# Kernel optimization log

Measured on AMD Instinct MI355X. Metric: run time of the kernel, lower is better.

## Reference

```python
import jax, jax.numpy as jnp
import numpy as np

N_NODES = 50000
N_EDGES = 800000
HEADS = 4
NEG_SLOPE = 0.2  # DGL GATConv default and act1 slope


def _gat_layer(x, src, dst, W, al, ar, b, n_nodes, heads, dh):
    # x: [N, Fin] -> proj: [N, H, Dh]
    proj = (x @ W).reshape(n_nodes, heads, dh)
    el = jnp.einsum('nhd,hd->nh', proj, al)  # [N, H]
    er = jnp.einsum('nhd,hd->nh', proj, ar)  # [N, H]
    e = jax.nn.leaky_relu(el[src] + er[dst], NEG_SLOPE)  # [E, H]
    # segment softmax over incoming edges of each dst node
    m = jax.ops.segment_max(e, dst, num_segments=n_nodes)
    m = jnp.where(jnp.isfinite(m), m, jnp.zeros_like(m))
    ex = jnp.exp(e - m[dst])
    s = jax.ops.segment_sum(ex, dst, num_segments=n_nodes)
    alpha = ex / (s[dst] + 1e-9)  # [E, H]
    msg = proj[src] * alpha[:, :, None]  # [E, H, Dh]
    out = jax.ops.segment_sum(msg, dst, num_segments=n_nodes)  # [N, H, Dh]
    return out.reshape(n_nodes, heads * dh) + b


def setup_inputs() -> dict:
    key = jax.random.key(0)
    ks = jax.random.split(key, 10)
    d = {
        'init_emb': jax.random.normal(ks[0], (N_NODES, 300), jnp.float32) * 0.1,
        'W1': jax.random.normal(ks[1], (300, 400), jnp.float32) * (1.0 / np.sqrt(300)),
        'al1': jax.random.normal(ks[2], (HEADS, 100), jnp.float32) * 0.1,
        'ar1': jax.random.normal(ks[3], (HEADS, 100), jnp.float32) * 0.1,
        'b1': jnp.zeros((400,), jnp.float32),
        'W2': jax.random.normal(ks[4], (400, 512), jnp.float32) * (1.0 / np.sqrt(400)),
        'al2': jax.random.normal(ks[5], (HEADS, 128), jnp.float32) * 0.1,
        'ar2': jax.random.normal(ks[6], (HEADS, 128), jnp.float32) * 0.1,
        'b2': jnp.zeros((512,), jnp.float32),
        'src': jax.random.randint(ks[7], (N_EDGES,), 0, N_NODES, jnp.int32),
        'dst': jax.random.randint(ks[8], (N_EDGES,), 0, N_NODES, jnp.int32),
    }
    return d


def reference(init_emb, W1, al1, ar1, b1, W2, al2, ar2, b2, src, dst):
    x = _gat_layer(init_emb, src, dst, W1, al1, ar1, b1, N_NODES, HEADS, 100)  # [N, 400]
    x = jax.nn.leaky_relu(x, NEG_SLOPE)  # act1
    x = _gat_layer(x, src, dst, W2, al2, ar2, b2, N_NODES, HEADS, 128)  # [N, 512]
    return x
```

## Files before the change

### kernel.cpp

```cpp
#include <hip/hip_runtime.h>
#include <math.h>
#include <stdint.h>

#define NN 50000
#define NE 800000
#define HEADS 4
#define MPAD 50048

typedef __attribute__((ext_vector_type(8))) short bf16x8;
typedef __attribute__((ext_vector_type(4))) float f32x4;

__device__ __forceinline__ uint32_t bf16rne(float x) {
  uint32_t b = __float_as_uint(x);
  return (b + 0x7FFFu + ((b >> 16) & 1u)) >> 16;
}
__device__ __forceinline__ float bflo(uint32_t v) {
  return __uint_as_float(v << 16);
}
__device__ __forceinline__ float bfhi(uint32_t v) {
  return __uint_as_float(v & 0xFFFF0000u);
}

__global__ void hist_kernel(const int* __restrict__ dst, int* __restrict__ counts, int n) {
  int i = blockIdx.x * blockDim.x + threadIdx.x;
  if (i < n) atomicAdd(&counts[dst[i]], 1);
}

__global__ void scan_kernel(const int* __restrict__ counts, int* __restrict__ row_ptr, int n) {
  __shared__ int wsum[16];
  const int lane = threadIdx.x & 63;
  const int w = threadIdx.x >> 6;
  int carry = 0;
  for (int start = 0; start < n; start += 1024) {
    int i = start + (int)threadIdx.x;
    int v = (i < n) ? counts[i] : 0;
    int x = v;
#pragma unroll
    for (int off = 1; off < 64; off <<= 1) {
      int t = __shfl_up(x, off);
      if (lane >= off) x += t;
    }
    if (lane == 63) wsum[w] = x;
    __syncthreads();
    if (w == 0 && lane < 16) {
      int s = wsum[lane];
#pragma unroll
      for (int off = 1; off < 16; off <<= 1) {
        int t = __shfl_up(s, off);
        if (lane >= off) s += t;
      }
      wsum[lane] = s;
    }
    __syncthreads();
    int woff = (w > 0) ? wsum[w - 1] : 0;
    int incl = x + woff;
    if (i < n) row_ptr[i] = carry + incl - v;
    carry += wsum[15];
    __syncthreads();
  }
  if (threadIdx.x == 0) row_ptr[n] = carry;
}

__global__ void scatter_kernel(const int* __restrict__ dst, const int* __restrict__ src,
                               const int* __restrict__ row_ptr, int* __restrict__ cursor,
                               int* __restrict__ srcs, int n) {
  int i = blockIdx.x * blockDim.x + threadIdx.x;
  if (i < n) {
    int d = dst[i];
    int pos = atomicAdd(&cursor[d], 1);
    srcs[row_ptr[d] + pos] = src[i];
  }
}

__global__ void presplit_pairs(const float* __restrict__ X, unsigned short* __restrict__ X2,
                               int M, int K, int ksteps) {
  const int m = blockIdx.y;
  const int t = threadIdx.x;
  if (t >= ksteps * 4) return;
  const int s = t >> 2, q = t & 3;
  const int kb = s * 32 + q * 8;
  float v[8];
#pragma unroll
  for (int j = 0; j < 8; ++j) {
    int k = kb + j;
    v[j] = (m < M && k < K) ? X[(size_t)m * K + k] : 0.f;
  }
  uint32_t hi[8], lo[8];
#pragma unroll
  for (int j = 0; j < 8; ++j) {
    hi[j] = bf16rne(v[j]);
    float back = __uint_as_float(hi[j] << 16);
    lo[j] = bf16rne(v[j] - back);
  }
  uint4 hp, lp;
  hp.x = hi[0] | (hi[1] << 16);
  hp.y = hi[2] | (hi[3] << 16);
  hp.z = hi[4] | (hi[5] << 16);
  hp.w = hi[6] | (hi[7] << 16);
  lp.x = lo[0] | (lo[1] << 16);
  lp.y = lo[2] | (lo[3] << 16);
  lp.z = lo[4] | (lo[5] << 16);
  lp.w = lo[6] | (lo[7] << 16);
  char* rowp = (char*)X2 + (size_t)m * (ksteps * 128) + s * 128;
  const int x = m & 7;
  *(uint4*)(rowp + ((q ^ x) << 4)) = hp;
  *(uint4*)(rowp + (((4 | q) ^ x) << 4)) = lp;
}

__global__ void presplit_pairs_b(const float* __restrict__ W, unsigned short* __restrict__ B2,
                                 int K, int N, int ksteps) {
  const int n = blockIdx.y;
  const int t = threadIdx.x;
  if (t >= ksteps * 4) return;
  const int s = t >> 2, q = t & 3;
  const int kb = s * 32 + q * 8;
  float v[8];
#pragma unroll
  for (int j = 0; j < 8; ++j) {
    int k = kb + j;
    v[j] = (n < N && k < K) ? W[(size_t)k * N + n] : 0.f;
  }
  uint32_t hi[8], lo[8];
#pragma unroll
  for (int j = 0; j < 8; ++j) {
    hi[j] = bf16rne(v[j]);
    float back = __uint_as_float(hi[j] << 16);
    lo[j] = bf16rne(v[j] - back);
  }
  uint4 hp, lp;
  hp.x = hi[0] | (hi[1] << 16);
  hp.y = hi[2] | (hi[3] << 16);
  hp.z = hi[4] | (hi[5] << 16);
  hp.w = hi[6] | (hi[7] << 16);
  lp.x = lo[0] | (lo[1] << 16);
  lp.y = lo[2] | (lo[3] << 16);
  lp.z = lo[4] | (lo[5] << 16);
  lp.w = lo[6] | (lo[7] << 16);
  char* rowp = (char*)B2 + (size_t)n * (ksteps * 128) + s * 128;
  const int x = n & 7;
  *(uint4*)(rowp + ((q ^ x) << 4)) = hp;
  *(uint4*)(rowp + (((4 | q) ^ x) << 4)) = lp;
}

__global__ __launch_bounds__(256, 2) void gemm_pairs(
    const unsigned short* __restrict__ A2, const unsigned short* __restrict__ B2,
    unsigned short* __restrict__ Ch, int M, int ksteps, int NstR, int RSc,
    int DHR, int DHP, int magic) {
  __shared__ unsigned short As[8192];
  __shared__ unsigned short Bs[8192];
  const int tid = threadIdx.x;
  const int w = tid >> 6, lane = tid & 63;
  const int wr = w >> 1, wc = w & 1;
  const int ln = lane & 15, quad = lane >> 4;
  const int m0 = blockIdx.y * 128, n0 = blockIdx.x * 128;
  const long strideB = (long)ksteps * 128;

  f32x4 acc[4][4];
#pragma unroll
  for (int mi = 0; mi < 4; ++mi)
#pragma unroll
    for (int ni = 0; ni < 4; ++ni) acc[mi][ni] = (f32x4){0.f, 0.f, 0.f, 0.f};

  const int xa = ln & 7;
  const int gA0 = (quad ^ xa) << 4, gA1 = ((4 | quad) ^ xa) << 4;

  for (int s = 0; s < ksteps; ++s) {
    const long sb = (long)s * 128;
#pragma unroll
    for (int j = 0; j < 4; ++j) {
      const int t16 = w * 4 + j;
      const int row = t16 * 8 + (lane >> 3);
      const int gran = lane & 7;
      const char* gpA = (const char*)A2 + (size_t)(m0 + row) * strideB + sb + gran * 16;
      const char* gpB = (const char*)B2 + (size_t)(n0 + row) * strideB + sb + gran * 16;
      __builtin_amdgcn_global_load_lds(
          (const __attribute__((address_space(1))) void*)gpA,
          (__attribute__((address_space(3))) void*)((char*)As + t16 * 1024), 16, 0, 0);
      __builtin_amdgcn_global_load_lds(
          (const __attribute__((address_space(1))) void*)gpB,
          (__attribute__((address_space(3))) void*)((char*)Bs + t16 * 1024), 16, 0, 0);
    }
    __syncthreads();
    bf16x8 ah[4], alo[4], bh[4], blo[4];
#pragma unroll
    for (int mi = 0; mi < 4; ++mi) {
      const int rA = wr * 64 + mi * 16 + ln;
      ah[mi] = *(const bf16x8*)((const char*)As + rA * 128 + gA0);
      alo[mi] = *(const bf16x8*)((const char*)As + rA * 128 + gA1);
    }
#pragma unroll
    for (int ni = 0; ni < 4; ++ni) {
      const int rB = wc * 64 + ni * 16 + ln;
      bh[ni] = *(const bf16x8*)((const char*)Bs + rB * 128 + gA0);
      blo[ni] = *(const bf16x8*)((const char*)Bs + rB * 128 + gA1);
    }
#pragma unroll
    for (int mi = 0; mi < 4; ++mi)
#pragma unroll
      for (int ni = 0; ni < 4; ++ni)
        acc[mi][ni] = __builtin_amdgcn_mfma_f32_16x16x32_bf16(ah[mi], bh[ni], acc[mi][ni], 0, 0, 0);
#pragma unroll
    for (int mi = 0; mi < 4; ++mi)
#pragma unroll
      for (int ni = 0; ni < 4; ++ni)
        acc[mi][ni] = __builtin_amdgcn_mfma_f32_16x16x32_bf16(ah[mi], blo[ni], acc[mi][ni], 0, 0, 0);
#pragma unroll
    for (int mi = 0; mi < 4; ++mi)
#pragma unroll
      for (int ni = 0; ni < 4; ++ni)
        acc[mi][ni] = __builtin_amdgcn_mfma_f32_16x16x32_bf16(alo[mi], bh[ni], acc[mi][ni], 0, 0, 0);
    __syncthreads();
  }
#pragma unroll
  for (int mi = 0; mi < 4; ++mi) {
#pragma unroll
    for (int r = 0; r < 4; ++r) {
      int gm = m0 + wr * 64 + mi * 16 + quad * 4 + r;
      if (gm < M) {
        unsigned short* crow = Ch + (size_t)gm * RSc;
#pragma unroll
        for (int ni = 0; ni < 4; ++ni) {
          int gn = n0 + wc * 64 + ni * 16 + ln;
          if (gn < NstR) {
            int h = (gn * magic) >> 12;
            int col = h * DHP + (gn - h * DHR);
            crow[col] = (unsigned short)bf16rne(acc[mi][ni][r]);
          }
        }
      }
    }
  }
}

template <int DHR, int DHP>
__global__ void el_er_kernel(const unsigned short* __restrict__ projh,
                             const float* __restrict__ al, const float* __restrict__ ar,
                             float* __restrict__ el, float* __restrict__ er) {
  int t = blockIdx.x * blockDim.x + threadIdx.x;
  if (t >= NN * HEADS) return;
  int h = t & (HEADS - 1);
  int n = t >> 2;
  const unsigned short* pr = projh + (size_t)n * (HEADS * DHP) + (size_t)h * DHP;
  const float* alh = al + h * DHR;
  const float* arh = ar + h * DHR;
  float sl = 0.f, sr = 0.f;
#pragma unroll 4
  for (int d = 0; d < DHR; d += 4) {
    uint2 pv = *(const uint2*)&pr[d];
    float p0 = bflo(pv.x), p1 = bfhi(pv.x), p2 = bflo(pv.y), p3 = bfhi(pv.y);
    float4 av = *(const float4*)&alh[d];
    float4 rv = *(const float4*)&arh[d];
    sl += p0 * av.x + p1 * av.y + p2 * av.z + p3 * av.w;
    sr += p0 * rv.x + p1 * rv.y + p2 * rv.z + p3 * rv.w;
  }
  el[t] = sl;
  er[t] = sr;
}

template <int DHP, int DHR, bool ACT>
__global__ __launch_bounds__(256) void aggregate2(
    const unsigned short* __restrict__ projh, const float* __restrict__ el,
    const float* __restrict__ er, const float* __restrict__ bias,
    const int* __restrict__ row_ptr, const int* __restrict__ srcs,
    float* __restrict__ out) {
  constexpr int LPH = DHP / 8;
  constexpr int RS = HEADS * DHP * 2;
  const int node = blockIdx.x * 4 + (threadIdx.x >> 6);
  if (node >= NN) return;
  const int lane = threadIdx.x & 63;
  const int beg = row_ptr[node], end = row_ptr[node + 1];
  const int e16 = lane >> 2, hp = lane & 3;
  const float er_p = er[node * 4 + hp];
  int head;
  if constexpr (LPH == 16) head = lane >> 4;
  else head = (lane * 5) >> 6;
  const int u = lane - head * LPH;
  const int laneByte = head * (DHP * 2) + u * 16;
  const bool active = lane < 4 * LPH;
  const char* pb = (const char*)projh;

  float bv[8];
  const int d0 = u * 8;
#pragma unroll
  for (int j = 0; j < 8; ++j)
    bv[j] = (active && d0 + j < DHR) ? bias[head * DHR + d0 + j] : 0.f;

  float acc[8];
#pragma unroll
  for (int j = 0; j < 8; ++j) acc[j] = 0.f;
  float lsum = 0.f;

  int i = beg;
  int rem = end - beg;
  int sE = 0;
  float elv = 0.f;
  if (rem > 0 && e16 < rem) {
    sE = srcs[i + e16];
    elv = el[sE * 4 + hp];
  }
  while (rem > 0) {
    const int take = rem < 16 ? rem : 16;
    float ev = elv + er_p;
    ev = fmaxf(ev, 0.2f * ev);
    const float pv_ = (e16 < take) ? __expf(ev) : 0.f;
    const int off_ = sE * RS;
    const int i2 = i + take;
    const int rem2 = rem - take;
    int sEn = 0;
    float elvn = 0.f;
    if (rem2 > 0 && e16 < rem2) {
      sEn = srcs[i2 + e16];
      elvn = el[sEn * 4 + hp];
    }
    if (take == 16) {
#pragma unroll
      for (int e = 0; e < 16; ++e) {
        const int sl = e * 4 + head;
        const float pv = __shfl(pv_, sl);
        const int off = __shfl(off_, sl);
        uint4 q = *(const uint4*)(pb + (uint32_t)(off + laneByte));
        lsum += pv;
        acc[0] += pv * bflo(q.x);
        acc[1] += pv * bfhi(q.x);
        acc[2] += pv * bflo(q.y);
        acc[3] += pv * bfhi(q.y);
        acc[4] += pv * bflo(q.z);
        acc[5] += pv * bfhi(q.z);
        acc[6] += pv * bflo(q.w);
        acc[7] += pv * bfhi(q.w);
      }
    } else {
      for (int e = 0; e < take; ++e) {
        const int sl = e * 4 + head;
        const float pv = __shfl(pv_, sl);
        const int off = __shfl(off_, sl);
        uint4 q = *(const uint4*)(pb + (uint32_t)(off + laneByte));
        lsum += pv;
        acc[0] += pv * bflo(q.x);
        acc[1] += pv * bfhi(q.x);
        acc[2] += pv * bflo(q.y);
        acc[3] += pv * bfhi(q.y);
        acc[4] += pv * bflo(q.z);
        acc[5] += pv * bfhi(q.z);
        acc[6] += pv * bflo(q.w);
        acc[7] += pv * bfhi(q.w);
      }
    }
    sE = sEn;
    elv = elvn;
    i = i2;
    rem = rem2;
  }

  const float inv = 1.f / (lsum + 1e-9f);
  if (active) {
    float o[8];
#pragma unroll
    for (int j = 0; j < 8; ++j) {
      float v = acc[j] * inv + bv[j];
      if (ACT) v = (v > 0.f) ? v : 0.2f * v;
      o[j] = v;
    }
    float* orow = out + (size_t)node * (HEADS * DHR) + head * DHR + d0;
    *(float4*)orow = make_float4(o[0], o[1], o[2], o[3]);
    if (d0 + 7 < DHR) *(float4*)(orow + 4) = make_float4(o[4], o[5], o[6], o[7]);
  }
}

extern "C" void kernel_launch(void* const* d_in, const int* in_sizes, int n_in,
                              void* d_out, int out_size, void* d_ws, size_t ws_size,
                              hipStream_t stream) {
  const float* init_emb = (const float*)d_in[0];
  const float* W1 = (const float*)d_in[1];
  const float* al1 = (const float*)d_in[2];
  const float* ar1 = (const float*)d_in[3];
  const float* b1 = (const float*)d_in[4];
  const float* W2 = (const float*)d_in[5];
  const float* al2 = (const float*)d_in[6];
  const float* ar2 = (const float*)d_in[7];
  const float* b2 = (const float*)d_in[8];
  const int* src = (const int*)d_in[9];
  const int* dst = (const int*)d_in[10];
  float* out = (float*)d_out;

  char* ws = (char*)d_ws;
  size_t off = 0;
  auto alloc = [&](size_t bytes) {
    void* p = ws + off;
    off += (bytes + 255) & ~((size_t)255);
    return p;
  };
  unsigned short* projh = (unsigned short*)alloc((size_t)NN * 512 * 2);
  float* x1 = (float*)alloc((size_t)NN * 400 * 4);
  float* el = (float*)alloc((size_t)NN * HEADS * 4);
  float* er = (float*)alloc((size_t)NN * HEADS * 4);
  unsigned short* B2 = (unsigned short*)alloc((size_t)512 * 13 * 128);
  int* row_ptr = (int*)alloc((size_t)(NN + 1) * 4);
  int* counts = (int*)alloc((size_t)NN * 4);
  int* srcs = (int*)alloc((size_t)NE * 4);
  unsigned short* A2 = (unsigned short*)d_out;

  hipMemsetAsync(counts, 0, (size_t)NN * 4, stream);
  hist_kernel<<<(NE + 255) / 256, 256, 0, stream>>>(dst, counts, NE);
  scan_kernel<<<1, 1024, 0, stream>>>(counts, row_ptr, NN);
  hipMemsetAsync(counts, 0, (size_t)NN * 4, stream);
  scatter_kernel<<<(NE + 255) / 256, 256, 0, stream>>>(dst, src, row_ptr, counts, srcs, NE);

  presplit_pairs<<<dim3(1, MPAD), 64, 0, stream>>>(init_emb, A2, NN, 300, 10);
  presplit_pairs_b<<<dim3(1, 512), 64, 0, stream>>>(W1, B2, 300, 400, 10);
  gemm_pairs<<<dim3(4, MPAD / 128), 256, 0, stream>>>(A2, B2, projh, NN, 10, 400, 416, 100, 104, 41);
  el_er_kernel<100, 104><<<(NN * HEADS + 255) / 256, 256, 0, stream>>>(projh, al1, ar1, el, er);
  aggregate2<104, 100, true><<<(NN + 3) / 4, 256, 0, stream>>>(projh, el, er, b1, row_ptr, srcs, x1);

  presplit_pairs<<<dim3(1, MPAD), 64, 0, stream>>>(x1, A2, NN, 400, 13);
  presplit_pairs_b<<<dim3(1, 512), 64, 0, stream>>>(W2, B2, 400, 512, 13);
  gemm_pairs<<<dim3(4, MPAD / 128), 256, 0, stream>>>(A2, B2, projh, NN, 13, 512, 512, 128, 128, 32);
  el_er_kernel<128, 128><<<(NN * HEADS + 255) / 256, 256, 0, stream>>>(projh, al2, ar2, el, er);
  aggregate2<128, 128, false><<<(NN + 3) / 4, 256, 0, stream>>>(projh, el, er, b2, row_ptr, srcs, out);
}
```

Baseline: 797.4 us.

## Fuse layer-1 output bf16 split into aggregation and repack W2 for padded heads

```diff
diff --git a/kernel.cpp b/kernel.cpp
--- a/kernel.cpp
+++ b/kernel.cpp
@@ -73,38 +73,42 @@
 }
 
 __global__ void presplit_pairs(const float* __restrict__ X, unsigned short* __restrict__ X2,
-                               int M, int K, int ksteps) {
-  const int m = blockIdx.y;
-  const int t = threadIdx.x;
-  if (t >= ksteps * 4) return;
+                               int M, int Mpad, int K, int ksteps) {
+  const int wid = blockIdx.x * (blockDim.x >> 6) + (threadIdx.x >> 6);
+  const int nw = gridDim.x * (blockDim.x >> 6);
+  const int t = threadIdx.x & 63;
   const int s = t >> 2, q = t & 3;
+  const bool act = t < ksteps * 4;
   const int kb = s * 32 + q * 8;
-  float v[8];
-#pragma unroll
-  for (int j = 0; j < 8; ++j) {
-    int k = kb + j;
-    v[j] = (m < M && k < K) ? X[(size_t)m * K + k] : 0.f;
-  }
-  uint32_t hi[8], lo[8];
-#pragma unroll
-  for (int j = 0; j < 8; ++j) {
-    hi[j] = bf16rne(v[j]);
-    float back = __uint_as_float(hi[j] << 16);
-    lo[j] = bf16rne(v[j] - back);
-  }
-  uint4 hp, lp;
-  hp.x = hi[0] | (hi[1] << 16);
-  hp.y = hi[2] | (hi[3] << 16);
-  hp.z = hi[4] | (hi[5] << 16);
-  hp.w = hi[6] | (hi[7] << 16);
-  lp.x = lo[0] | (lo[1] << 16);
-  lp.y = lo[2] | (lo[3] << 16);
-  lp.z = lo[4] | (lo[5] << 16);
-  lp.w = lo[6] | (lo[7] << 16);
-  char* rowp = (char*)X2 + (size_t)m * (ksteps * 128) + s * 128;
-  const int x = m & 7;
-  *(uint4*)(rowp + ((q ^ x) << 4)) = hp;
-  *(uint4*)(rowp + (((4 | q) ^ x) << 4)) = lp;
+  for (int m = wid; m < Mpad; m += nw) {
+    if (!act) continue;
+    float v[8];
+#pragma unroll
+    for (int j = 0; j < 8; ++j) {
+      int k = kb + j;
+      v[j] = (m < M && k < K) ? X[(size_t)m * K + k] : 0.f;
+    }
+    uint32_t hi[8], lo[8];
+#pragma unroll
+    for (int j = 0; j < 8; ++j) {
+      hi[j] = bf16rne(v[j]);
+      float back = __uint_as_float(hi[j] << 16);
+      lo[j] = bf16rne(v[j] - back);
+    }
+    uint4 hp, lp;
+    hp.x = hi[0] | (hi[1] << 16);
+    hp.y = hi[2] | (hi[3] << 16);
+    hp.z = hi[4] | (hi[5] << 16);
+    hp.w = hi[6] | (hi[7] << 16);
+    lp.x = lo[0] | (lo[1] << 16);
+    lp.y = lo[2] | (lo[3] << 16);
+    lp.z = lo[4] | (lo[5] << 16);
+    lp.w = lo[6] | (lo[7] << 16);
+    char* rowp = (char*)X2 + (size_t)m * (ksteps * 128) + s * 128;
+    const int x = m & 7;
+    *(uint4*)(rowp + ((q ^ x) << 4)) = hp;
+    *(uint4*)(rowp + (((4 | q) ^ x) << 4)) = lp;
+  }
 }
 
 __global__ void presplit_pairs_b(const float* __restrict__ W, unsigned short* __restrict__ B2,
@@ -137,6 +141,42 @@
   lp.z = lo[4] | (lo[5] << 16);
   lp.w = lo[6] | (lo[7] << 16);
   char* rowp = (char*)B2 + (size_t)n * (ksteps * 128) + s * 128;
+  const int x = n & 7;
+  *(uint4*)(rowp + ((q ^ x) << 4)) = hp;
+  *(uint4*)(rowp + (((4 | q) ^ x) << 4)) = lp;
+}
+
+__global__ void presplit_pairs_b2(const float* __restrict__ W, unsigned short* __restrict__ B2) {
+  const int n = blockIdx.y;
+  const int t = threadIdx.x;
+  if (t >= 52) return;
+  const int s = t >> 2, q = t & 3;
+  const int kb = s * 32 + q * 8;
+  float v[8];
+#pragma unroll
+  for (int j = 0; j < 8; ++j) {
+    int kp = kb + j;
+    int h = kp / 104;
+    int d = kp - h * 104;
+    v[j] = (d < 100) ? W[(size_t)(h * 100 + d) * 512 + n] : 0.f;
+  }
+  uint32_t hi[8], lo[8];
+#pragma unroll
+  for (int j = 0; j < 8; ++j) {
+    hi[j] = bf16rne(v[j]);
+    float back = __uint_as_float(hi[j] << 16);
+    lo[j] = bf16rne(v[j] - back);
+  }
+  uint4 hp, lp;
+  hp.x = hi[0] | (hi[1] << 16);
+  hp.y = hi[2] | (hi[3] << 16);
+  hp.z = hi[4] | (hi[5] << 16);
+  hp.w = hi[6] | (hi[7] << 16);
+  lp.x = lo[0] | (lo[1] << 16);
+  lp.y = lo[2] | (lo[3] << 16);
+  lp.z = lo[4] | (lo[5] << 16);
+  lp.w = lo[6] | (lo[7] << 16);
+  char* rowp = (char*)B2 + (size_t)n * 1664 + s * 128;
   const int x = n & 7;
   *(uint4*)(rowp + ((q ^ x) << 4)) = hp;
   *(uint4*)(rowp + (((4 | q) ^ x) << 4)) = lp;
@@ -257,12 +297,12 @@
   er[t] = sr;
 }
 
-template <int DHP, int DHR, bool ACT>
+template <int DHP, int DHR, bool ACT, bool EMIT>
 __global__ __launch_bounds__(256) void aggregate2(
     const unsigned short* __restrict__ projh, const float* __restrict__ el,
     const float* __restrict__ er, const float* __restrict__ bias,
     const int* __restrict__ row_ptr, const int* __restrict__ srcs,
-    float* __restrict__ out) {
+    float* __restrict__ out, unsigned short* __restrict__ a2) {
   constexpr int LPH = DHP / 8;
   constexpr int RS = HEADS * DHP * 2;
   const int node = blockIdx.x * 4 + (threadIdx.x >> 6);
@@ -275,8 +315,8 @@
   if constexpr (LPH == 16) head = lane >> 4;
   else head = (lane * 5) >> 6;
   const int u = lane - head * LPH;
-  const int laneByte = head * (DHP * 2) + u * 16;
   const bool active = lane < 4 * LPH;
+  const int laneByte = active ? head * (DHP * 2) + u * 16 : 0;
   const char* pb = (const char*)projh;
 
   float bv[8];
@@ -359,11 +399,35 @@
     for (int j = 0; j < 8; ++j) {
       float v = acc[j] * inv + bv[j];
       if (ACT) v = (v > 0.f) ? v : 0.2f * v;
-      o[j] = v;
-    }
-    float* orow = out + (size_t)node * (HEADS * DHR) + head * DHR + d0;
-    *(float4*)orow = make_float4(o[0], o[1], o[2], o[3]);
-    if (d0 + 7 < DHR) *(float4*)(orow + 4) = make_float4(o[4], o[5], o[6], o[7]);
+      o[j] = (d0 + j < DHR) ? v : 0.f;
+    }
+    if constexpr (EMIT) {
+      uint32_t hi8[8], lo8[8];
+#pragma unroll
+      for (int j = 0; j < 8; ++j) {
+        hi8[j] = bf16rne(o[j]);
+        float back = __uint_as_float(hi8[j] << 16);
+        lo8[j] = bf16rne(o[j] - back);
+      }
+      uint4 hpx, lpx;
+      hpx.x = hi8[0] | (hi8[1] << 16);
+      hpx.y = hi8[2] | (hi8[3] << 16);
+      hpx.z = hi8[4] | (hi8[5] << 16);
+      hpx.w = hi8[6] | (hi8[7] << 16);
+      lpx.x = lo8[0] | (lo8[1] << 16);
+      lpx.y = lo8[2] | (lo8[3] << 16);
+      lpx.z = lo8[4] | (lo8[5] << 16);
+      lpx.w = lo8[6] | (lo8[7] << 16);
+      const int kp = head * DHP + u * 8;
+      const int s2 = kp >> 5, q2 = (kp >> 3) & 3, xs = node & 7;
+      char* rb = (char*)a2 + (size_t)node * 1664 + s2 * 128;
+      *(uint4*)(rb + ((q2 ^ xs) << 4)) = hpx;
+      *(uint4*)(rb + (((4 | q2) ^ xs) << 4)) = lpx;
+    } else {
+      float* orow = out + (size_t)node * (HEADS * DHR) + head * DHR + d0;
+      *(float4*)orow = make_float4(o[0], o[1], o[2], o[3]);
+      if (d0 + 7 < DHR) *(float4*)(orow + 4) = make_float4(o[4], o[5], o[6], o[7]);
+    }
   }
 }
 
@@ -391,7 +455,6 @@
     return p;
   };
   unsigned short* projh = (unsigned short*)alloc((size_t)NN * 512 * 2);
-  float* x1 = (float*)alloc((size_t)NN * 400 * 4);
   float* el = (float*)alloc((size_t)NN * HEADS * 4);
   float* er = (float*)alloc((size_t)NN * HEADS * 4);
   unsigned short* B2 = (unsigned short*)alloc((size_t)512 * 13 * 128);
@@ -406,15 +469,16 @@
   hipMemsetAsync(counts, 0, (size_t)NN * 4, stream);
   scatter_kernel<<<(NE + 255) / 256, 256, 0, stream>>>(dst, src, row_ptr, counts, srcs, NE);
 
-  presplit_pairs<<<dim3(1, MPAD), 64, 0, stream>>>(init_emb, A2, NN, 300, 10);
+  presplit_pairs<<<1024, 256, 0, stream>>>(init_emb, A2, NN, MPAD, 300, 10);
   presplit_pairs_b<<<dim3(1, 512), 64, 0, stream>>>(W1, B2, 300, 400, 10);
   gemm_pairs<<<dim3(4, MPAD / 128), 256, 0, stream>>>(A2, B2, projh, NN, 10, 400, 416, 100, 104, 41);
   el_er_kernel<100, 104><<<(NN * HEADS + 255) / 256, 256, 0, stream>>>(projh, al1, ar1, el, er);
-  aggregate2<104, 100, true><<<(NN + 3) / 4, 256, 0, stream>>>(projh, el, er, b1, row_ptr, srcs, x1);
-
-  presplit_pairs<<<dim3(1, MPAD), 64, 0, stream>>>(x1, A2, NN, 400, 13);
-  presplit_pairs_b<<<dim3(1, 512), 64, 0, stream>>>(W2, B2, 400, 512, 13);
+  aggregate2<104, 100, true, true><<<(NN + 3) / 4, 256, 0, stream>>>(projh, el, er, b1, row_ptr,
+                                                                     srcs, nullptr, A2);
+
+  presplit_pairs_b2<<<dim3(1, 512), 64, 0, stream>>>(W2, B2);
   gemm_pairs<<<dim3(4, MPAD / 128), 256, 0, stream>>>(A2, B2, projh, NN, 13, 512, 512, 128, 128, 32);
   el_er_kernel<128, 128><<<(NN * HEADS + 255) / 256, 256, 0, stream>>>(projh, al2, ar2, el, er);
-  aggregate2<128, 128, false><<<(NN + 3) / 4, 256, 0, stream>>>(projh, el, er, b2, row_ptr, srcs, out);
-}
+  aggregate2<128, 128, false, false><<<(NN + 3) / 4, 256, 0, stream>>>(projh, el, er, b2, row_ptr,
+                                                                       srcs, out, nullptr);
+}
```

New measurement: 774.4 us. -2.9%, faster.

## Fuse layer-1 aggregation with bf16 pair split and merge preprocessing kernels

Applied to the files above, without the earlier changes.

```diff
diff --git a/kernel.cpp b/kernel.cpp
--- a/kernel.cpp
+++ b/kernel.cpp
@@ -21,70 +21,7 @@
   return __uint_as_float(v & 0xFFFF0000u);
 }
 
-__global__ void hist_kernel(const int* __restrict__ dst, int* __restrict__ counts, int n) {
-  int i = blockIdx.x * blockDim.x + threadIdx.x;
-  if (i < n) atomicAdd(&counts[dst[i]], 1);
-}
-
-__global__ void scan_kernel(const int* __restrict__ counts, int* __restrict__ row_ptr, int n) {
-  __shared__ int wsum[16];
-  const int lane = threadIdx.x & 63;
-  const int w = threadIdx.x >> 6;
-  int carry = 0;
-  for (int start = 0; start < n; start += 1024) {
-    int i = start + (int)threadIdx.x;
-    int v = (i < n) ? counts[i] : 0;
-    int x = v;
-#pragma unroll
-    for (int off = 1; off < 64; off <<= 1) {
-      int t = __shfl_up(x, off);
-      if (lane >= off) x += t;
-    }
-    if (lane == 63) wsum[w] = x;
-    __syncthreads();
-    if (w == 0 && lane < 16) {
-      int s = wsum[lane];
-#pragma unroll
-      for (int off = 1; off < 16; off <<= 1) {
-        int t = __shfl_up(s, off);
-        if (lane >= off) s += t;
-      }
-      wsum[lane] = s;
-    }
-    __syncthreads();
-    int woff = (w > 0) ? wsum[w - 1] : 0;
-    int incl = x + woff;
-    if (i < n) row_ptr[i] = carry + incl - v;
-    carry += wsum[15];
-    __syncthreads();
-  }
-  if (threadIdx.x == 0) row_ptr[n] = carry;
-}
-
-__global__ void scatter_kernel(const int* __restrict__ dst, const int* __restrict__ src,
-                               const int* __restrict__ row_ptr, int* __restrict__ cursor,
-                               int* __restrict__ srcs, int n) {
-  int i = blockIdx.x * blockDim.x + threadIdx.x;
-  if (i < n) {
-    int d = dst[i];
-    int pos = atomicAdd(&cursor[d], 1);
-    srcs[row_ptr[d] + pos] = src[i];
-  }
-}
-
-__global__ void presplit_pairs(const float* __restrict__ X, unsigned short* __restrict__ X2,
-                               int M, int K, int ksteps) {
-  const int m = blockIdx.y;
-  const int t = threadIdx.x;
-  if (t >= ksteps * 4) return;
-  const int s = t >> 2, q = t & 3;
-  const int kb = s * 32 + q * 8;
-  float v[8];
-#pragma unroll
-  for (int j = 0; j < 8; ++j) {
-    int k = kb + j;
-    v[j] = (m < M && k < K) ? X[(size_t)m * K + k] : 0.f;
-  }
+__device__ __forceinline__ void pair_write(const float v[8], char* rowp, int q, int x) {
   uint32_t hi[8], lo[8];
 #pragma unroll
   for (int j = 0; j < 8; ++j) {
@@ -101,45 +38,107 @@
   lp.y = lo[2] | (lo[3] << 16);
   lp.z = lo[4] | (lo[5] << 16);
   lp.w = lo[6] | (lo[7] << 16);
-  char* rowp = (char*)X2 + (size_t)m * (ksteps * 128) + s * 128;
-  const int x = m & 7;
   *(uint4*)(rowp + ((q ^ x) << 4)) = hp;
   *(uint4*)(rowp + (((4 | q) ^ x) << 4)) = lp;
 }
 
-__global__ void presplit_pairs_b(const float* __restrict__ W, unsigned short* __restrict__ B2,
-                                 int K, int N, int ksteps) {
-  const int n = blockIdx.y;
-  const int t = threadIdx.x;
-  if (t >= ksteps * 4) return;
+__global__ void hist_kernel(const int* __restrict__ dst, int* __restrict__ counts, int n) {
+  int i = blockIdx.x * blockDim.x + threadIdx.x;
+  if (i < n) atomicAdd(&counts[dst[i]], 1);
+}
+
+__global__ void scan_kernel(const int* __restrict__ counts, int* __restrict__ row_ptr,
+                            int* __restrict__ cursor, int n) {
+  __shared__ int wsum[16];
+  const int lane = threadIdx.x & 63;
+  const int w = threadIdx.x >> 6;
+  int carry = 0;
+  for (int start = 0; start < n; start += 1024) {
+    int i = start + (int)threadIdx.x;
+    int v = (i < n) ? counts[i] : 0;
+    int x = v;
+#pragma unroll
+    for (int off = 1; off < 64; off <<= 1) {
+      int t = __shfl_up(x, off);
+      if (lane >= off) x += t;
+    }
+    if (lane == 63) wsum[w] = x;
+    __syncthreads();
+    if (w == 0 && lane < 16) {
+      int s = wsum[lane];
+#pragma unroll
+      for (int off = 1; off < 16; off <<= 1) {
+        int t = __shfl_up(s, off);
+        if (lane >= off) s += t;
+      }
+      wsum[lane] = s;
+    }
+    __syncthreads();
+    int woff = (w > 0) ? wsum[w - 1] : 0;
+    int incl = x + woff;
+    if (i < n) {
+      int val = carry + incl - v;
+      row_ptr[i] = val;
+      cursor[i] = val;
+    }
+    carry += wsum[15];
+    __syncthreads();
+  }
+  if (threadIdx.x == 0) row_ptr[n] = carry;
+}
+
+__global__ void scatter_kernel(const int* __restrict__ dst, const int* __restrict__ src,
+                               int* __restrict__ cursor, int* __restrict__ srcs, int n) {
+  int i = blockIdx.x * blockDim.x + threadIdx.x;
+  if (i < n) {
+    int pos = atomicAdd(&cursor[dst[i]], 1);
+    srcs[pos] = src[i];
+  }
+}
+
+__global__ void prepare_kernel(const float* __restrict__ X, unsigned short* __restrict__ A2,
+                               const float* __restrict__ W1, unsigned short* __restrict__ B2a,
+                               const float* __restrict__ W2, unsigned short* __restrict__ B2b) {
+  const int bid = blockIdx.x;
+  const int wv = threadIdx.x >> 6;
+  const int t = threadIdx.x & 63;
   const int s = t >> 2, q = t & 3;
   const int kb = s * 32 + q * 8;
-  float v[8];
-#pragma unroll
-  for (int j = 0; j < 8; ++j) {
-    int k = kb + j;
-    v[j] = (n < N && k < K) ? W[(size_t)k * N + n] : 0.f;
-  }
-  uint32_t hi[8], lo[8];
-#pragma unroll
-  for (int j = 0; j < 8; ++j) {
-    hi[j] = bf16rne(v[j]);
-    float back = __uint_as_float(hi[j] << 16);
-    lo[j] = bf16rne(v[j] - back);
-  }
-  uint4 hp, lp;
-  hp.x = hi[0] | (hi[1] << 16);
-  hp.y = hi[2] | (hi[3] << 16);
-  hp.z = hi[4] | (hi[5] << 16);
-  hp.w = hi[6] | (hi[7] << 16);
-  lp.x = lo[0] | (lo[1] << 16);
-  lp.y = lo[2] | (lo[3] << 16);
-  lp.z = lo[4] | (lo[5] << 16);
-  lp.w = lo[6] | (lo[7] << 16);
-  char* rowp = (char*)B2 + (size_t)n * (ksteps * 128) + s * 128;
-  const int x = n & 7;
-  *(uint4*)(rowp + ((q ^ x) << 4)) = hp;
-  *(uint4*)(rowp + (((4 | q) ^ x) << 4)) = lp;
+  if (bid < 1024) {
+    if (t >= 40) return;
+    const int nw = 1024 * 4;
+    for (int m = bid * 4 + wv; m < MPAD; m += nw) {
+      float v[8];
+#pragma unroll
+      for (int j = 0; j < 8; ++j) {
+        int k = kb + j;
+        v[j] = (m < NN && k < 300) ? X[(size_t)m * 300 + k] : 0.f;
+      }
+      pair_write(v, (char*)A2 + (size_t)m * 1280 + s * 128, q, m & 7);
+    }
+  } else if (bid < 1152) {
+    if (t >= 40) return;
+    const int n = (bid - 1024) * 4 + wv;
+    float v[8];
+#pragma unroll
+    for (int j = 0; j < 8; ++j) {
+      int k = kb + j;
+      v[j] = (n < 400 && k < 300) ? W1[(size_t)k * 400 + n] : 0.f;
+    }
+    pair_write(v, (char*)B2a + (size_t)n * 1280 + s * 128, q, n & 7);
+  } else {
+    if (t >= 52) return;
+    const int n = (bid - 1152) * 4 + wv;
+    float v[8];
+#pragma unroll
+    for (int j = 0; j < 8; ++j) {
+      int kp = kb + j;
+      int h = kp / 104;
+      int d = kp - h * 104;
+      v[j] = (d < 100) ? W2[(size_t)(h * 100 + d) * 512 + n] : 0.f;
+    }
+    pair_write(v, (char*)B2b + (size_t)n * 1664 + s * 128, q, n & 7);
+  }
 }
 
 __global__ __launch_bounds__(256, 2) void gemm_pairs(
@@ -257,26 +256,24 @@
   er[t] = sr;
 }
 
-template <int DHP, int DHR, bool ACT>
-__global__ __launch_bounds__(256) void aggregate2(
+template <int DHP, int DHR, bool ACT, bool EMIT>
+__global__ __launch_bounds__(256) void aggregate4(
     const unsigned short* __restrict__ projh, const float* __restrict__ el,
     const float* __restrict__ er, const float* __restrict__ bias,
     const int* __restrict__ row_ptr, const int* __restrict__ srcs,
-    float* __restrict__ out) {
+    float* __restrict__ out, unsigned short* __restrict__ a2) {
   constexpr int LPH = DHP / 8;
   constexpr int RS = HEADS * DHP * 2;
-  const int node = blockIdx.x * 4 + (threadIdx.x >> 6);
-  if (node >= NN) return;
   const int lane = threadIdx.x & 63;
-  const int beg = row_ptr[node], end = row_ptr[node + 1];
+  const int wid = blockIdx.x * 4 + (threadIdx.x >> 6);
+  const int nw = gridDim.x * 4;
   const int e16 = lane >> 2, hp = lane & 3;
-  const float er_p = er[node * 4 + hp];
   int head;
   if constexpr (LPH == 16) head = lane >> 4;
   else head = (lane * 5) >> 6;
   const int u = lane - head * LPH;
-  const int laneByte = head * (DHP * 2) + u * 16;
   const bool active = lane < 4 * LPH;
+  const int laneByte = active ? head * (DHP * 2) + u * 16 : 0;
   const char* pb = (const char*)projh;
 
   float bv[8];
@@ -285,85 +282,96 @@
   for (int j = 0; j < 8; ++j)
     bv[j] = (active && d0 + j < DHR) ? bias[head * DHR + d0 + j] : 0.f;
 
-  float acc[8];
-#pragma unroll
-  for (int j = 0; j < 8; ++j) acc[j] = 0.f;
-  float lsum = 0.f;
-
-  int i = beg;
-  int rem = end - beg;
-  int sE = 0;
-  float elv = 0.f;
-  if (rem > 0 && e16 < rem) {
-    sE = srcs[i + e16];
-    elv = el[sE * 4 + hp];
-  }
-  while (rem > 0) {
-    const int take = rem < 16 ? rem : 16;
-    float ev = elv + er_p;
-    ev = fmaxf(ev, 0.2f * ev);
-    const float pv_ = (e16 < take) ? __expf(ev) : 0.f;
-    const int off_ = sE * RS;
-    const int i2 = i + take;
-    const int rem2 = rem - take;
-    int sEn = 0;
-    float elvn = 0.f;
-    if (rem2 > 0 && e16 < rem2) {
-      sEn = srcs[i2 + e16];
-      elvn = el[sEn * 4 + hp];
-    }
-    if (take == 16) {
-#pragma unroll
-      for (int e = 0; e < 16; ++e) {
-        const int sl = e * 4 + head;
-        const float pv = __shfl(pv_, sl);
-        const int off = __shfl(off_, sl);
-        uint4 q = *(const uint4*)(pb + (uint32_t)(off + laneByte));
-        lsum += pv;
-        acc[0] += pv * bflo(q.x);
-        acc[1] += pv * bfhi(q.x);
-        acc[2] += pv * bflo(q.y);
-        acc[3] += pv * bfhi(q.y);
-        acc[4] += pv * bflo(q.z);
-        acc[5] += pv * bfhi(q.z);
-        acc[6] += pv * bflo(q.w);
-        acc[7] += pv * bfhi(q.w);
-      }
-    } else {
-      for (int e = 0; e < take; ++e) {
-        const int sl = e * 4 + head;
-        const float pv = __shfl(pv_, sl);
-        const int off = __shfl(off_, sl);
-        uint4 q = *(const uint4*)(pb + (uint32_t)(off + laneByte));
-        lsum += pv;
-        acc[0] += pv * bflo(q.x);
-        acc[1] += pv * bfhi(q.x);
-        acc[2] += pv * bflo(q.y);
-        acc[3] += pv * bfhi(q.y);
-        acc[4] += pv * bflo(q.z);
-        acc[5] += pv * bfhi(q.z);
-        acc[6] += pv * bflo(q.w);
-        acc[7] += pv * bfhi(q.w);
-      }
-    }
-    sE = sEn;
-    elv = elvn;
-    i = i2;
-    rem = rem2;
-  }
-
-  const float inv = 1.f / (lsum + 1e-9f);
-  if (active) {
-    float o[8];
-#pragma unroll
-    for (int j = 0; j < 8; ++j) {
-      float v = acc[j] * inv + bv[j];
-      if (ACT) v = (v > 0.f) ? v : 0.2f * v;
-      o[j] = v;
-    }
-    float* orow = out + (size_t)node * (HEADS * DHR) + head * DHR + d0;
-    *(float4*)orow = make_float4(o[0], o[1], o[2], o[3]);
-    if (d0 + 7 < DHR) *(float4*)(orow + 4) = make_float4(o[4], o[5], o[6], o[7]);
+  for (int node = wid; node < NN; node += nw) {
+    const int beg = row_ptr[node], end = row_ptr[node + 1];
+    const float er_p = er[node * 4 + hp];
+
+    float acc[8];
+#pragma unroll
+    for (int j = 0; j < 8; ++j) acc[j] = 0.f;
+    float lsum = 0.f;
+
+    int i = beg;
+    int rem = end - beg;
+    int sE = 0;
+    float elv = 0.f;
+    if (rem > 0 && e16 < rem) {
+      sE = srcs[i + e16];
+      elv = el[sE * 4 + hp];
+    }
+    while (rem > 0) {
+      const int take = rem < 16 ? rem : 16;
+      float ev = elv + er_p;
+      ev = fmaxf(ev, 0.2f * ev);
+      const float pv_ = (e16 < take) ? __expf(ev) : 0.f;
+      const int off_ = sE * RS;
+      const int i2 = i + take;
+      const int rem2 = rem - take;
+      int sEn = 0;
+      float elvn = 0.f;
+      if (rem2 > 0 && e16 < rem2) {
+        sEn = srcs[i2 + e16];
+        elvn = el[sEn * 4 + hp];
+      }
+      if (take == 16) {
+#pragma unroll
+        for (int e = 0; e < 16; ++e) {
+          const int sl = e * 4 + head;
+          const float pv = __shfl(pv_, sl);
+          const int off = __shfl(off_, sl);
+          uint4 q = *(const uint4*)(pb + (uint32_t)(off + laneByte));
+          lsum += pv;
+          acc[0] += pv * bflo(q.x);
+          acc[1] += pv * bfhi(q.x);
+          acc[2] += pv * bflo(q.y);
+          acc[3] += pv * bfhi(q.y);
+          acc[4] += pv * bflo(q.z);
+          acc[5] += pv * bfhi(q.z);
+          acc[6] += pv * bflo(q.w);
+          acc[7] += pv * bfhi(q.w);
+        }
+      } else {
+        for (int e = 0; e < take; ++e) {
+          const int sl = e * 4 + head;
+          const float pv = __shfl(pv_, sl);
+          const int off = __shfl(off_, sl);
+          uint4 q = *(const uint4*)(pb + (uint32_t)(off + laneByte));
+          lsum += pv;
+          acc[0] += pv * bflo(q.x);
+          acc[1] += pv * bfhi(q.x);
+          acc[2] += pv * bflo(q.y);
+          acc[3] += pv * bfhi(q.y);
+          acc[4] += pv * bflo(q.z);
+          acc[5] += pv * bfhi(q.z);
+          acc[6] += pv * bflo(q.w);
+          acc[7] += pv * bfhi(q.w);
+        }
+      }
+      sE = sEn;
+      elv = elvn;
+      i = i2;
+      rem = rem2;
+    }
+
+    const float inv = 1.f / (lsum + 1e-9f);
+    if (active) {
+      float o[8];
+#pragma unroll
+      for (int j = 0; j < 8; ++j) {
+        float v = acc[j] * inv + bv[j];
+        if (ACT) v = (v > 0.f) ? v : 0.2f * v;
+        o[j] = (d0 + j < DHR) ? v : 0.f;
+      }
+      if constexpr (EMIT) {
+        const int kp = head * DHP + u * 8;
+        const int s2 = kp >> 5, q2 = (kp >> 3) & 3;
+        pair_write(o, (char*)a2 + (size_t)node * 1664 + s2 * 128, q2, node & 7);
+      } else {
+        float* orow = out + (size_t)node * (HEADS * DHR) + head * DHR + d0;
+        *(float4*)orow = make_float4(o[0], o[1], o[2], o[3]);
+        if (d0 + 7 < DHR) *(float4*)(orow + 4) = make_float4(o[4], o[5], o[6], o[7]);
+      }
+    }
   }
 }
 
@@ -391,30 +399,30 @@
     return p;
   };
   unsigned short* projh = (unsigned short*)alloc((size_t)NN * 512 * 2);
-  float* x1 = (float*)alloc((size_t)NN * 400 * 4);
   float* el = (float*)alloc((size_t)NN * HEADS * 4);
   float* er = (float*)alloc((size_t)NN * HEADS * 4);
-  unsigned short* B2 = (unsigned short*)alloc((size_t)512 * 13 * 128);
+  unsigned short* B2a = (unsigned short*)alloc((size_t)512 * 10 * 128);
+  unsigned short* B2b = (unsigned short*)alloc((size_t)512 * 13 * 128);
   int* row_ptr = (int*)alloc((size_t)(NN + 1) * 4);
   int* counts = (int*)alloc((size_t)NN * 4);
+  int* cursor = (int*)alloc((size_t)NN * 4);
   int* srcs = (int*)alloc((size_t)NE * 4);
   unsigned short* A2 = (unsigned short*)d_out;
 
+  prepare_kernel<<<1280, 256, 0, stream>>>(init_emb, A2, W1, B2a, W2, B2b);
+
   hipMemsetAsync(counts, 0, (size_t)NN * 4, stream);
   hist_kernel<<<(NE + 255) / 256, 256, 0, stream>>>(dst, counts, NE);
-  scan_kernel<<<1, 1024, 0, stream>>>(counts, row_ptr, NN);
-  hipMemsetAsync(counts, 0, (size_t)NN * 4, stream);
-  scatter_kernel<<<(NE + 255) / 256, 256, 0, stream>>>(dst, src, row_ptr, counts, srcs, NE);
-
-  presplit_pairs<<<dim3(1, MPAD), 64, 0, stream>>>(init_emb, A2, NN, 300, 10);
-  presplit_pairs_b<<<dim3(1, 512), 64, 0, stream>>>(W1, B2, 300, 400, 10);
-  gemm_pairs<<<dim3(4, MPAD / 128), 256, 0, stream>>>(A2, B2, projh, NN, 10, 400, 416, 100, 104, 41);
+  scan_kernel<<<1, 1024, 0, stream>>>(counts, row_ptr, cursor, NN);
+  scatter_kernel<<<(NE + 255) / 256, 256, 0, stream>>>(dst, src, cursor, srcs, NE);
+
+  gemm_pairs<<<dim3(4, MPAD / 128), 256, 0, stream>>>(A2, B2a, projh, NN, 10, 400, 416, 100, 104, 41);
   el_er_kernel<100, 104><<<(NN * HEADS + 255) / 256, 256, 0, stream>>>(projh, al1, ar1, el, er);
-  aggregate2<104, 100, true><<<(NN + 3) / 4, 256, 0, stream>>>(projh, el, er, b1, row_ptr, srcs, x1);
-
-  presplit_pairs<<<dim3(1, MPAD), 64, 0, stream>>>(x1, A2, NN, 400, 13);
-  presplit_pairs_b<<<dim3(1, 512), 64, 0, stream>>>(W2, B2, 400, 512, 13);
-  gemm_pairs<<<dim3(4, MPAD / 128), 256, 0, stream>>>(A2, B2, projh, NN, 13, 512, 512, 128, 128, 32);
+  aggregate4<104, 100, true, true><<<2048, 256, 0, stream>>>(projh, el, er, b1, row_ptr,
+                                                             srcs, nullptr, A2);
+
+  gemm_pairs<<<dim3(4, MPAD / 128), 256, 0, stream>>>(A2, B2b, projh, NN, 13, 512, 512, 128, 128, 32);
   el_er_kernel<128, 128><<<(NN * HEADS + 255) / 256, 256, 0, stream>>>(projh, al2, ar2, el, er);
-  aggregate2<128, 128, false><<<(NN + 3) / 4, 256, 0, stream>>>(projh, el, er, b2, row_ptr, srcs, out);
-}
+  aggregate4<128, 128, false, false><<<2048, 256, 0, stream>>>(projh, el, er, b2, row_ptr,
+                                                               srcs, out, nullptr);
+}
```

After: 775.3 us. 1.03x faster.
